# Kernel tuning notes

Hardware: AMD Instinct MI355X
Metric: run time of the kernel (lower is better)

## Reference

```python
import jax, jax.numpy as jnp
from jax import lax
import numpy as np

CLIP = 20.0  # DeepSpeech clipped-ReLU bound


def setup_inputs() -> dict:
    key = jax.random.key(0)
    k1, k2, k3 = jax.random.split(key, 3)
    B, T, F, U_ = 32, 800, 161, 1024
    inputs = jax.random.normal(k1, (B, T, F), dtype=jnp.float32)
    W = jax.random.normal(k2, (F, U_), dtype=jnp.float32) * 0.05
    U = jax.random.normal(k3, (U_, U_), dtype=jnp.float32) * 0.02
    b = jnp.zeros((U_,), dtype=jnp.float32)
    return {"inputs": inputs, "W": W, "U": U, "b": b}


def reference(inputs, W, U, b):
    # inputs: [B, T, F]; shared cell weights for both directions.
    B = inputs.shape[0]
    units = U.shape[0]
    # Precompute input projection for all timesteps: [T, B, units]
    xW = (jnp.einsum('btf,fu->btu', inputs, W) + b).transpose(1, 0, 2)
    h0 = jnp.zeros((B, units), dtype=inputs.dtype)

    def step(h, x):
        h = jnp.minimum(jax.nn.relu(x + h @ U), CLIP)
        return h, None

    hf, _ = lax.scan(step, h0, xW)                 # final state, forward direction
    hb, _ = lax.scan(step, h0, xW, reverse=True)   # final state, go_backwards
    return hf + hb
```

## Files before the change

### kernel.cpp

```cpp
#include <hip/hip_runtime.h>
#include <hip/hip_bf16.h>

#define T_STEPS 800
#define BATCH   32
#define FEAT    161
#define UNITS   1024
#define CLIPV   20.0f

typedef __attribute__((ext_vector_type(8))) short short8;
typedef __attribute__((ext_vector_type(4))) float f32x4;
typedef unsigned short u16;
typedef unsigned int   u32;
typedef unsigned long long u64;

__device__ __forceinline__ float bf16_f(u16 u) {
    return __uint_as_float(((u32)u) << 16);
}
__device__ __forceinline__ u16 bf16_rn(float x) {
    __hip_bfloat16 b = __float2bfloat16(x);
    return *(u16*)&b;
}
__device__ __forceinline__ u64 ld_agent_u64(const u64* p) {
    return __hip_atomic_load(p, __ATOMIC_RELAXED, __HIP_MEMORY_SCOPE_AGENT);
}
__device__ __forceinline__ float ld_agent_f(const float* p) {
    return __hip_atomic_load(p, __ATOMIC_RELAXED, __HIP_MEMORY_SCOPE_AGENT);
}
__device__ __forceinline__ void xchg_agent_u32(u32* p, u32 v) {
    (void)__hip_atomic_exchange(p, v, __ATOMIC_RELAXED, __HIP_MEMORY_SCOPE_AGENT);
}
__device__ __forceinline__ void xchg_agent_f(float* p, float v) {
    xchg_agent_u32((u32*)p, __float_as_uint(v));
}
__device__ __forceinline__ short8 ld_agent_b16x8(const u16* p) {
    union { u64 q[2]; short8 v; } u;
    u.q[0] = ld_agent_u64((const u64*)p);
    u.q[1] = ld_agent_u64((const u64*)p + 1);
    return u.v;
}

__global__ __launch_bounds__(256) void init_ws(float* hbuf, u32* flags) {
    int gid = blockIdx.x * 256 + threadIdx.x;
    for (int i = gid; i < 2 * 64 * UNITS; i += 64 * 256) hbuf[i] = 0.f;
    if (gid < 256) flags[gid] = 0u;
}

__global__ __launch_bounds__(256) void u_split_t(const float* __restrict__ U,
                                                 u16* __restrict__ Ut1,
                                                 u16* __restrict__ Ut2,
                                                 u16* __restrict__ Ut3) {
    __shared__ float tile[32][33];
    int bx = blockIdx.x, by = blockIdx.y;
    int lx = threadIdx.x & 31;
    int ly4 = (threadIdx.x >> 5) * 4;
    #pragma unroll
    for (int j = 0; j < 4; ++j)
        tile[ly4 + j][lx] = U[(size_t)(by * 32 + ly4 + j) * UNITS + bx * 32 + lx];
    __syncthreads();
    #pragma unroll
    for (int j = 0; j < 4; ++j) {
        float x = tile[lx][ly4 + j];
        size_t o = (size_t)(bx * 32 + ly4 + j) * UNITS + by * 32 + lx;
        u16 s1 = bf16_rn(x);  float r1 = x - bf16_f(s1);
        u16 s2 = bf16_rn(r1); float r2 = r1 - bf16_f(s2);
        u16 s3 = bf16_rn(r2);
        Ut1[o] = s1; Ut2[o] = s2; Ut3[o] = s3;
    }
}

__global__ __launch_bounds__(256) void xw_gemm(const float* __restrict__ inp,
                                               const float* __restrict__ W,
                                               const float* __restrict__ bias,
                                               float* __restrict__ xW) {
    __shared__ float xs[8 * FEAT];
    int t = blockIdx.x;
    int b0 = blockIdx.y * 8;
    int tid = threadIdx.x;

    for (int i = tid; i < 8 * FEAT; i += 256) {
        int j = i / FEAT;
        int f = i - j * FEAT;
        xs[i] = inp[((size_t)(b0 + j) * T_STEPS + t) * FEAT + f];
    }
    __syncthreads();

    float bv[4];
    #pragma unroll
    for (int c = 0; c < 4; ++c) bv[c] = bias[tid + c * 256];

    float acc[8][4];
    #pragma unroll
    for (int j = 0; j < 8; ++j)
        #pragma unroll
        for (int c = 0; c < 4; ++c) acc[j][c] = bv[c];

    for (int f = 0; f < FEAT; ++f) {
        float w0 = W[(size_t)f * UNITS + tid];
        float w1 = W[(size_t)f * UNITS + tid + 256];
        float w2 = W[(size_t)f * UNITS + tid + 512];
        float w3 = W[(size_t)f * UNITS + tid + 768];
        #pragma unroll
        for (int j = 0; j < 8; ++j) {
            float xv = xs[j * FEAT + f];
            acc[j][0] += xv * w0;
            acc[j][1] += xv * w1;
            acc[j][2] += xv * w2;
            acc[j][3] += xv * w3;
        }
    }

    #pragma unroll
    for (int j = 0; j < 8; ++j)
        #pragma unroll
        for (int c = 0; c < 4; ++c)
            xW[((size_t)t * BATCH + b0 + j) * UNITS + tid + c * 256] = acc[j][c];
}

__global__ __launch_bounds__(512) void rnn_scan(
        const float* __restrict__ xW,
        const u16* __restrict__ Ut1, const u16* __restrict__ Ut2,
        const u16* __restrict__ Ut3,
        float* __restrict__ hbuf, u32* __restrict__ flags,
        float* __restrict__ out) {
    __shared__ f32x4 red[14][64];

    const int tid  = threadIdx.x;
    const int bk   = blockIdx.x;
    const int lane = tid & 63;
    const int kq   = tid >> 6;
    const int quad = lane >> 4;
    const int n16  = lane & 15;
    const int rg   = bk & 3;
    const int ug   = bk >> 2;
    const int R0   = rg * 16;
    const int u0   = ug * 32;
    const int dir  = rg >> 1;

    short8 bfr[4][2][3];
    #pragma unroll
    for (int ks = 0; ks < 4; ++ks) {
        const int koff = kq * 128 + ks * 32 + quad * 8;
        #pragma unroll
        for (int nq = 0; nq < 2; ++nq) {
            const size_t ub = (size_t)(u0 + nq * 16 + n16) * UNITS + koff;
            bfr[ks][nq][0] = ld_agent_b16x8(Ut1 + ub);
            bfr[ks][nq][1] = ld_agent_b16x8(Ut2 + ub);
            bfr[ks][nq][2] = ld_agent_b16x8(Ut3 + ub);
        }
    }

    const size_t HS = (size_t)64 * UNITS;
    u32* myflag = flags + rg * 32 + ug;
    const u64* srcflag = (const u64*)(flags + rg * 32 + kq * 4);

    for (int t = 0; t < T_STEPS; ++t) {
        const size_t sb = (size_t)(t & 1) * HS;
        const size_t db = sb ^ HS;

        float xp[2][4];
        if (kq == 0) {
            const int xt = dir ? (T_STEPS - 1 - t) : t;
            #pragma unroll
            for (int nq = 0; nq < 2; ++nq)
                #pragma unroll
                for (int j = 0; j < 4; ++j) {
                    const int b = (R0 + quad * 4 + j) & 31;
                    xp[nq][j] = xW[(size_t)xt * (BATCH * UNITS) +
                                   (size_t)b * UNITS + u0 + nq * 16 + n16];
                }
        }

        const u32 tgt = (u32)t;
        for (;;) {
            u64 qa = ld_agent_u64(srcflag);
            u64 qb = ld_agent_u64(srcflag + 1);
            u32 f0 = (u32)qa, f1 = (u32)(qa >> 32);
            u32 f2 = (u32)qb, f3 = (u32)(qb >> 32);
            if (f0 >= tgt && f1 >= tgt && f2 >= tgt && f3 >= tgt) break;
        }

        f32x4 acc[2][2] = {{{0.f,0.f,0.f,0.f},{0.f,0.f,0.f,0.f}},
                           {{0.f,0.f,0.f,0.f},{0.f,0.f,0.f,0.f}}};
        #pragma unroll
        for (int ks = 0; ks < 4; ++ks) {
            const float* ap = hbuf + sb + (size_t)(R0 + n16) * UNITS +
                              kq * 128 + ks * 32 + quad * 8;
            union { u64 q[4]; float f[8]; u32 u[8]; } hv;
            hv.q[0] = ld_agent_u64((const u64*)ap);
            hv.q[1] = ld_agent_u64((const u64*)ap + 1);
            hv.q[2] = ld_agent_u64((const u64*)ap + 2);
            hv.q[3] = ld_agent_u64((const u64*)ap + 3);
            short8 a1, a2, a3;
            #pragma unroll
            for (int j = 0; j < 8; ++j) {
                float x = hv.f[j];
                u16 s1 = (u16)(hv.u[j] >> 16);
                float r1 = x - bf16_f(s1);
                u16 s2 = (u16)(__float_as_uint(r1) >> 16);
                float r2 = r1 - bf16_f(s2);
                u16 s3 = (u16)(__float_as_uint(r2) >> 16);
                a1[j] = (short)s1; a2[j] = (short)s2; a3[j] = (short)s3;
            }
            #pragma unroll
            for (int nq = 0; nq < 2; ++nq) {
                acc[nq][0] = __builtin_amdgcn_mfma_f32_16x16x32_bf16(a1, bfr[ks][nq][0], acc[nq][0], 0, 0, 0);
                acc[nq][1] = __builtin_amdgcn_mfma_f32_16x16x32_bf16(a2, bfr[ks][nq][0], acc[nq][1], 0, 0, 0);
                acc[nq][0] = __builtin_amdgcn_mfma_f32_16x16x32_bf16(a1, bfr[ks][nq][1], acc[nq][0], 0, 0, 0);
                acc[nq][1] = __builtin_amdgcn_mfma_f32_16x16x32_bf16(a2, bfr[ks][nq][1], acc[nq][1], 0, 0, 0);
                acc[nq][0] = __builtin_amdgcn_mfma_f32_16x16x32_bf16(a1, bfr[ks][nq][2], acc[nq][0], 0, 0, 0);
                acc[nq][1] = __builtin_amdgcn_mfma_f32_16x16x32_bf16(a3, bfr[ks][nq][0], acc[nq][1], 0, 0, 0);
            }
        }
        f32x4 c0 = acc[0][0] + acc[0][1];
        f32x4 c1 = acc[1][0] + acc[1][1];

        if (kq) {
            red[(kq - 1) * 2 + 0][lane] = c0;
            red[(kq - 1) * 2 + 1][lane] = c1;
        }
        __syncthreads();
        if (kq == 0) {
            #pragma unroll
            for (int w = 0; w < 7; ++w) {
                c0 += red[w * 2 + 0][lane];
                c1 += red[w * 2 + 1][lane];
            }
            float* hdst = hbuf + db;
            #pragma unroll
            for (int nq = 0; nq < 2; ++nq)
                #pragma unroll
                for (int j = 0; j < 4; ++j) {
                    float a = (nq ? c1[j] : c0[j]) + xp[nq][j];
                    a = fminf(fmaxf(a, 0.f), CLIPV);
                    xchg_agent_f(hdst + (size_t)(R0 + quad * 4 + j) * UNITS +
                                 u0 + nq * 16 + n16, a);
                }
        }
        __syncthreads();
        if (tid == 0) xchg_agent_u32(myflag, (u32)(t + 1));
    }

    if (rg < 2) {
        const u32* bwd = flags + (rg + 2) * 32 + ug;
        while (__hip_atomic_load(bwd, __ATOMIC_RELAXED,
                                 __HIP_MEMORY_SCOPE_AGENT) < (u32)T_STEPS) {}
        const int r = tid >> 5, c = tid & 31;
        const int b = R0 + r;
        float hf = ld_agent_f(hbuf + (size_t)b * UNITS + u0 + c);
        float hb = ld_agent_f(hbuf + (size_t)(b + 32) * UNITS + u0 + c);
        out[(size_t)b * UNITS + u0 + c] = hf + hb;
    }
}

extern "C" void kernel_launch(void* const* d_in, const int* in_sizes, int n_in,
                              void* d_out, int out_size, void* d_ws, size_t ws_size,
                              hipStream_t stream) {
    const float* inp  = (const float*)d_in[0];
    const float* W    = (const float*)d_in[1];
    const float* U    = (const float*)d_in[2];
    const float* bias = (const float*)d_in[3];
    float* out = (float*)d_out;

    u16*   Ut1 = (u16*)d_ws;
    u16*   Ut2 = Ut1 + (size_t)UNITS * UNITS;
    u16*   Ut3 = Ut2 + (size_t)UNITS * UNITS;
    float* xW  = (float*)(Ut3 + (size_t)UNITS * UNITS);
    float* hbuf = xW + (size_t)T_STEPS * BATCH * UNITS;
    u32*   flags = (u32*)(hbuf + (size_t)2 * 64 * UNITS);

    init_ws<<<64, 256, 0, stream>>>(hbuf, flags);
    u_split_t<<<dim3(32, 32), 256, 0, stream>>>(U, Ut1, Ut2, Ut3);
    xw_gemm<<<dim3(800, 4), 256, 0, stream>>>(inp, W, bias, xW);

    void* args[] = {(void*)&xW, (void*)&Ut1, (void*)&Ut2, (void*)&Ut3,
                    (void*)&hbuf, (void*)&flags, (void*)&out};
    hipLaunchCooperativeKernel((const void*)rnn_scan, dim3(128), dim3(512),
                               args, 0, stream);
}
```

Before: 4.101 ms.

## Replace per-block step flags with timestep tags embedded in hidden-state words

Each hidden-state element is now stored as a 64-bit word: the three bf16 split components plus a 16-bit timestep tag. Consumers poll the data directly and can process whichever k-slices are ready, instead of waiting on separate producer flags. This removes the flag write/read round trip and the separate barrier step per timestep, and moves the bf16 three-way split from the consumer side to the producer. The cost is doubled hidden-state traffic, 64-bit atomic stores, and an all-lanes readiness check on every slice, with spin loops that sleep between polls.

```diff
diff --git a/kernel.cpp b/kernel.cpp
--- a/kernel.cpp
+++ b/kernel.cpp
@@ -23,14 +23,8 @@
 __device__ __forceinline__ u64 ld_agent_u64(const u64* p) {
     return __hip_atomic_load(p, __ATOMIC_RELAXED, __HIP_MEMORY_SCOPE_AGENT);
 }
-__device__ __forceinline__ float ld_agent_f(const float* p) {
-    return __hip_atomic_load(p, __ATOMIC_RELAXED, __HIP_MEMORY_SCOPE_AGENT);
-}
-__device__ __forceinline__ void xchg_agent_u32(u32* p, u32 v) {
+__device__ __forceinline__ void xchg_agent_u64(u64* p, u64 v) {
     (void)__hip_atomic_exchange(p, v, __ATOMIC_RELAXED, __HIP_MEMORY_SCOPE_AGENT);
-}
-__device__ __forceinline__ void xchg_agent_f(float* p, float v) {
-    xchg_agent_u32((u32*)p, __float_as_uint(v));
 }
 __device__ __forceinline__ short8 ld_agent_b16x8(const u16* p) {
     union { u64 q[2]; short8 v; } u;
@@ -39,10 +33,9 @@
     return u.v;
 }
 
-__global__ __launch_bounds__(256) void init_ws(float* hbuf, u32* flags) {
+__global__ __launch_bounds__(256) void init_ws(u64* hbuf) {
     int gid = blockIdx.x * 256 + threadIdx.x;
-    for (int i = gid; i < 2 * 64 * UNITS; i += 64 * 256) hbuf[i] = 0.f;
-    if (gid < 256) flags[gid] = 0u;
+    for (int i = gid; i < 2 * 64 * UNITS; i += 64 * 256) hbuf[i] = 0ull;
 }
 
 __global__ __launch_bounds__(256) void u_split_t(const float* __restrict__ U,
@@ -120,7 +113,7 @@
         const float* __restrict__ xW,
         const u16* __restrict__ Ut1, const u16* __restrict__ Ut2,
         const u16* __restrict__ Ut3,
-        float* __restrict__ hbuf, u32* __restrict__ flags,
+        u64* __restrict__ hbuf,
         float* __restrict__ out) {
     __shared__ f32x4 red[14][64];
 
@@ -150,8 +143,6 @@
     }
 
     const size_t HS = (size_t)64 * UNITS;
-    u32* myflag = flags + rg * 32 + ug;
-    const u64* srcflag = (const u64*)(flags + rg * 32 + kq * 4);
 
     for (int t = 0; t < T_STEPS; ++t) {
         const size_t sb = (size_t)(t & 1) * HS;
@@ -170,46 +161,48 @@
                 }
         }
 
+        const u64* abase = hbuf + sb + (size_t)(R0 + n16) * UNITS + kq * 128;
         const u32 tgt = (u32)t;
-        for (;;) {
-            u64 qa = ld_agent_u64(srcflag);
-            u64 qb = ld_agent_u64(srcflag + 1);
-            u32 f0 = (u32)qa, f1 = (u32)(qa >> 32);
-            u32 f2 = (u32)qb, f3 = (u32)(qb >> 32);
-            if (f0 >= tgt && f1 >= tgt && f2 >= tgt && f3 >= tgt) break;
-        }
-
         f32x4 acc[2][2] = {{{0.f,0.f,0.f,0.f},{0.f,0.f,0.f,0.f}},
                            {{0.f,0.f,0.f,0.f},{0.f,0.f,0.f,0.f}}};
-        #pragma unroll
-        for (int ks = 0; ks < 4; ++ks) {
-            const float* ap = hbuf + sb + (size_t)(R0 + n16) * UNITS +
-                              kq * 128 + ks * 32 + quad * 8;
-            union { u64 q[4]; float f[8]; u32 u[8]; } hv;
-            hv.q[0] = ld_agent_u64((const u64*)ap);
-            hv.q[1] = ld_agent_u64((const u64*)ap + 1);
-            hv.q[2] = ld_agent_u64((const u64*)ap + 2);
-            hv.q[3] = ld_agent_u64((const u64*)ap + 3);
-            short8 a1, a2, a3;
-            #pragma unroll
-            for (int j = 0; j < 8; ++j) {
-                float x = hv.f[j];
-                u16 s1 = (u16)(hv.u[j] >> 16);
-                float r1 = x - bf16_f(s1);
-                u16 s2 = (u16)(__float_as_uint(r1) >> 16);
-                float r2 = r1 - bf16_f(s2);
-                u16 s3 = (u16)(__float_as_uint(r2) >> 16);
-                a1[j] = (short)s1; a2[j] = (short)s2; a3[j] = (short)s3;
+        u32 pend = 0xFu;
+        while (pend) {
+            bool progress = false;
+            #pragma unroll
+            for (int ks = 0; ks < 4; ++ks) {
+                if (!(pend & (1u << ks))) continue;
+                const u64* ap = abase + ks * 32 + quad * 8;
+                u64 c0 = ld_agent_u64(ap);
+                if (!__all((int)((u32)(c0 >> 48) == tgt))) continue;
+                u64 w[8];
+                w[0] = c0;
+                #pragma unroll
+                for (int j = 1; j < 8; ++j) w[j] = ld_agent_u64(ap + j);
+                bool ok = true;
+                #pragma unroll
+                for (int j = 1; j < 8; ++j) ok &= ((u32)(w[j] >> 48) == tgt);
+                if (!__all((int)ok)) continue;
+                short8 a1, a2, a3;
+                #pragma unroll
+                for (int j = 0; j < 8; ++j) {
+                    const u32 lo = (u32)w[j];
+                    a1[j] = (short)(lo & 0xffffu);
+                    a2[j] = (short)(lo >> 16);
+                    a3[j] = (short)((u32)(w[j] >> 32) & 0xffffu);
+                }
+                #pragma unroll
+                for (int nq = 0; nq < 2; ++nq) {
+                    acc[nq][0] = __builtin_amdgcn_mfma_f32_16x16x32_bf16(a1, bfr[ks][nq][0], acc[nq][0], 0, 0, 0);
+                    acc[nq][1] = __builtin_amdgcn_mfma_f32_16x16x32_bf16(a2, bfr[ks][nq][0], acc[nq][1], 0, 0, 0);
+                    acc[nq][0] = __builtin_amdgcn_mfma_f32_16x16x32_bf16(a1, bfr[ks][nq][1], acc[nq][0], 0, 0, 0);
+                    acc[nq][1] = __builtin_amdgcn_mfma_f32_16x16x32_bf16(a2, bfr[ks][nq][1], acc[nq][1], 0, 0, 0);
+                    acc[nq][0] = __builtin_amdgcn_mfma_f32_16x16x32_bf16(a1, bfr[ks][nq][2], acc[nq][0], 0, 0, 0);
+                    acc[nq][1] = __builtin_amdgcn_mfma_f32_16x16x32_bf16(a3, bfr[ks][nq][0], acc[nq][1], 0, 0, 0);
+                }
+                pend &= ~(1u << ks);
+                progress = true;
             }
-            #pragma unroll
-            for (int nq = 0; nq < 2; ++nq) {
-                acc[nq][0] = __builtin_amdgcn_mfma_f32_16x16x32_bf16(a1, bfr[ks][nq][0], acc[nq][0], 0, 0, 0);
-                acc[nq][1] = __builtin_amdgcn_mfma_f32_16x16x32_bf16(a2, bfr[ks][nq][0], acc[nq][1], 0, 0, 0);
-                acc[nq][0] = __builtin_amdgcn_mfma_f32_16x16x32_bf16(a1, bfr[ks][nq][1], acc[nq][0], 0, 0, 0);
-                acc[nq][1] = __builtin_amdgcn_mfma_f32_16x16x32_bf16(a2, bfr[ks][nq][1], acc[nq][1], 0, 0, 0);
-                acc[nq][0] = __builtin_amdgcn_mfma_f32_16x16x32_bf16(a1, bfr[ks][nq][2], acc[nq][0], 0, 0, 0);
-                acc[nq][1] = __builtin_amdgcn_mfma_f32_16x16x32_bf16(a3, bfr[ks][nq][0], acc[nq][1], 0, 0, 0);
-            }
+            if (pend && !progress) __builtin_amdgcn_s_sleep(2);
         }
         f32x4 c0 = acc[0][0] + acc[0][1];
         f32x4 c1 = acc[1][0] + acc[1][1];
@@ -225,29 +218,47 @@
                 c0 += red[w * 2 + 0][lane];
                 c1 += red[w * 2 + 1][lane];
             }
-            float* hdst = hbuf + db;
+            u64* hdst = hbuf + db;
+            const u64 tagbits = ((u64)(u32)(t + 1)) << 48;
             #pragma unroll
             for (int nq = 0; nq < 2; ++nq)
                 #pragma unroll
                 for (int j = 0; j < 4; ++j) {
                     float a = (nq ? c1[j] : c0[j]) + xp[nq][j];
                     a = fminf(fmaxf(a, 0.f), CLIPV);
-                    xchg_agent_f(hdst + (size_t)(R0 + quad * 4 + j) * UNITS +
-                                 u0 + nq * 16 + n16, a);
+                    const u32 xb = __float_as_uint(a);
+                    const u16 s1 = (u16)(xb >> 16);
+                    const float r1 = a - bf16_f(s1);
+                    const u16 s2 = (u16)(__float_as_uint(r1) >> 16);
+                    const float r2 = r1 - bf16_f(s2);
+                    const u16 s3 = (u16)(__float_as_uint(r2) >> 16);
+                    const u64 wv = (u64)s1 | ((u64)s2 << 16) |
+                                   ((u64)s3 << 32) | tagbits;
+                    xchg_agent_u64(hdst + (size_t)(R0 + quad * 4 + j) * UNITS +
+                                   u0 + nq * 16 + n16, wv);
                 }
         }
         __syncthreads();
-        if (tid == 0) xchg_agent_u32(myflag, (u32)(t + 1));
     }
 
     if (rg < 2) {
-        const u32* bwd = flags + (rg + 2) * 32 + ug;
-        while (__hip_atomic_load(bwd, __ATOMIC_RELAXED,
-                                 __HIP_MEMORY_SCOPE_AGENT) < (u32)T_STEPS) {}
         const int r = tid >> 5, c = tid & 31;
         const int b = R0 + r;
-        float hf = ld_agent_f(hbuf + (size_t)b * UNITS + u0 + c);
-        float hb = ld_agent_f(hbuf + (size_t)(b + 32) * UNITS + u0 + c);
+        u64* pf = hbuf + (size_t)b * UNITS + u0 + c;
+        u64* pb = hbuf + (size_t)(b + 32) * UNITS + u0 + c;
+        u64 wf, wb;
+        for (;;) {
+            wf = ld_agent_u64(pf);
+            if ((u32)(wf >> 48) == (u32)T_STEPS) break;
+            __builtin_amdgcn_s_sleep(2);
+        }
+        for (;;) {
+            wb = ld_agent_u64(pb);
+            if ((u32)(wb >> 48) == (u32)T_STEPS) break;
+            __builtin_amdgcn_s_sleep(2);
+        }
+        const float hf = bf16_f((u16)wf) + bf16_f((u16)(wf >> 16)) + bf16_f((u16)(wf >> 32));
+        const float hb = bf16_f((u16)wb) + bf16_f((u16)(wb >> 16)) + bf16_f((u16)(wb >> 32));
         out[(size_t)b * UNITS + u0 + c] = hf + hb;
     }
 }
@@ -265,15 +276,14 @@
     u16*   Ut2 = Ut1 + (size_t)UNITS * UNITS;
     u16*   Ut3 = Ut2 + (size_t)UNITS * UNITS;
     float* xW  = (float*)(Ut3 + (size_t)UNITS * UNITS);
-    float* hbuf = xW + (size_t)T_STEPS * BATCH * UNITS;
-    u32*   flags = (u32*)(hbuf + (size_t)2 * 64 * UNITS);
-
-    init_ws<<<64, 256, 0, stream>>>(hbuf, flags);
+    u64*   hbuf = (u64*)(xW + (size_t)T_STEPS * BATCH * UNITS);
+
+    init_ws<<<64, 256, 0, stream>>>(hbuf);
     u_split_t<<<dim3(32, 32), 256, 0, stream>>>(U, Ut1, Ut2, Ut3);
     xw_gemm<<<dim3(800, 4), 256, 0, stream>>>(inp, W, bias, xW);
 
     void* args[] = {(void*)&xW, (void*)&Ut1, (void*)&Ut2, (void*)&Ut3,
-                    (void*)&hbuf, (void*)&flags, (void*)&out};
+                    (void*)&hbuf, (void*)&out};
     hipLaunchCooperativeKernel((const void*)rnn_scan, dim3(128), dim3(512),
                                args, 0, stream);
 }
```

Measured after the change: 7.158 ms. 1.75x slower.
